# Kernel tuning notes

Measured on AMD Instinct MI355X. Metric: run time of the kernel, lower is better.

## Reference

```python
import jax, jax.numpy as jnp
import numpy as np

C = 256          # embed_dim
NH = 8           # n_heads
NL = 4           # n_levels
NP = 4           # n_points
HD = C // NH     # head dim = 32
SS = np.array([[128, 128], [64, 64], [32, 32], [16, 16]], dtype=np.int64)  # (H_l, W_l)
LSI = np.concatenate([[0], np.cumsum(SS[:, 0] * SS[:, 1])[:-1]]).astype(np.int64)
LIN = int((SS[:, 0] * SS[:, 1]).sum())  # 21760
B = 2
LQ = LIN


def setup_inputs() -> dict:
    key = jax.random.key(0)
    ks = jax.random.split(key, 8)
    s = 0.02
    return {
        "query": jax.random.normal(ks[0], (B, LQ, C), jnp.float32),
        "reference_points": jax.random.uniform(ks[1], (B, LQ, NL, 2), dtype=jnp.float32),
        "input_flatten": jax.random.normal(ks[2], (B, LIN, C), jnp.float32),
        "W_value": jax.random.normal(ks[3], (C, C), jnp.float32) * s,
        "b_value": jnp.zeros((C,), jnp.float32),
        "W_off": jax.random.normal(ks[4], (C, NH * NL * NP * 2), jnp.float32) * s,
        "b_off": jnp.zeros((NH * NL * NP * 2,), jnp.float32),
        "W_attn": jax.random.normal(ks[5], (C, NH * NL * NP), jnp.float32) * s,
        "b_attn": jnp.zeros((NH * NL * NP,), jnp.float32),
        "W_out": jax.random.normal(ks[6], (C, C), jnp.float32) * s,
        "b_out": jnp.zeros((C,), jnp.float32),
        "input_spatial_shapes": jnp.asarray(SS),
        "input_level_start_index": jnp.asarray(LSI),
    }


def _msda(query, reference_points, input_flatten,
          W_value, b_value, W_off, b_off, W_attn, b_attn, W_out, b_out):
    N, Lq, _ = query.shape
    Lin = input_flatten.shape[1]
    # projections
    value = (input_flatten @ W_value + b_value).reshape(N, Lin, NH, HD)
    off = (query @ W_off + b_off).reshape(N, Lq, NH, NL, NP, 2)
    aw = jax.nn.softmax((query @ W_attn + b_attn).reshape(N, Lq, NH, NL * NP), axis=-1)
    aw = aw.reshape(N, Lq, NH, NL, NP)
    # normalizer is (W_l, H_l) per level
    norm = jnp.asarray(SS[:, ::-1].copy(), jnp.float32)  # (NL, 2)
    loc = reference_points[:, :, None, :, None, :] + off / norm[None, None, None, :, None, :]
    out = jnp.zeros((N, Lq, NH, HD), query.dtype)
    for l in range(NL):
        Hl, Wl = int(SS[l, 0]), int(SS[l, 1])
        st = int(LSI[l])
        v = value[:, st:st + Hl * Wl].transpose(0, 2, 1, 3)  # (N, NH, HW, HD)
        # grid_sample align_corners=False semantics: pixel = loc*size - 0.5
        x = loc[:, :, :, l, :, 0] * Wl - 0.5  # (N, Lq, NH, NP)
        y = loc[:, :, :, l, :, 1] * Hl - 0.5
        x0 = jnp.floor(x)
        y0 = jnp.floor(y)
        lw = x - x0
        lh = y - y0
        x0i = x0.astype(jnp.int32)
        y0i = y0.astype(jnp.int32)

        def corner(ix, iy, w):
            valid = (ix >= 0) & (ix < Wl) & (iy >= 0) & (iy < Hl)
            idx = jnp.clip(iy * Wl + ix, 0, Hl * Wl - 1)
            idx_t = idx.transpose(0, 2, 1, 3).reshape(N, NH, Lq * NP)
            g = jnp.take_along_axis(v, idx_t[:, :, :, None], axis=2)
            g = g.reshape(N, NH, Lq, NP, HD)
            wt = (w * valid).transpose(0, 2, 1, 3)  # (N, NH, Lq, NP)
            return g * wt[..., None]

        samp = (corner(x0i, y0i, (1 - lw) * (1 - lh))
                + corner(x0i + 1, y0i, lw * (1 - lh))
                + corner(x0i, y0i + 1, (1 - lw) * lh)
                + corner(x0i + 1, y0i + 1, lw * lh))
        out = out + jnp.einsum('nhqpd,nqhp->nqhd', samp, aw[:, :, :, l])
    return out.reshape(N, Lq, C) @ W_out + b_out


def reference(query, reference_points, input_flatten,
              W_value, b_value, W_off, b_off, W_attn, b_attn, W_out, b_out,
              input_spatial_shapes, input_level_start_index):
    return _msda(query, reference_points, input_flatten,
                 W_value, b_value, W_off, b_off, W_attn, b_attn, W_out, b_out)
```

## Files before the change

### kernel.cpp

```cpp
#include <hip/hip_runtime.h>

typedef unsigned short u16;
typedef unsigned int u32;
typedef short bf16x8 __attribute__((ext_vector_type(8)));
typedef float f32x4 __attribute__((ext_vector_type(4)));

#define LQ_ 21760
#define LIN_ 21760
#define CDIM 256
#define MROWS (2 * LQ_)

__device__ __forceinline__ u16 f2bf(float f) {
  u32 u;
  __builtin_memcpy(&u, &f, 4);
  u32 r = (u + 0x7fffu + ((u >> 16) & 1u)) >> 16;
  return (u16)r;
}
__device__ __forceinline__ u32 pack_bf16_rne(float a, float b) {
  return (u32)f2bf(a) | ((u32)f2bf(b) << 16);
}
__device__ __forceinline__ float bflo(u32 u) {
  u32 v = u << 16;
  float f;
  __builtin_memcpy(&f, &v, 4);
  return f;
}
__device__ __forceinline__ float bfhi(u32 u) {
  u32 v = u & 0xffff0000u;
  float f;
  __builtin_memcpy(&f, &v, 4);
  return f;
}

__device__ __forceinline__ void conv_one(const float* W0, const float* W1, u16* Wf,
                                         int N, int split, int blk, int t) {
  const int tid = blk * 256 + t;
  if (tid >= N * 32) return;
  const int n = tid >> 5, kcg = tid & 31;
  float w[8];
#pragma unroll
  for (int j = 0; j < 8; ++j) {
    const int k = kcg * 8 + j;
    w[j] = (n < split) ? W0[(size_t)k * split + n]
                       : W1[(size_t)k * (N - split) + (n - split)];
  }
  uint4 pk;
  pk.x = pack_bf16_rne(w[0], w[1]);
  pk.y = pack_bf16_rne(w[2], w[3]);
  pk.z = pack_bf16_rne(w[4], w[5]);
  pk.w = pack_bf16_rne(w[6], w[7]);
  const int ks = kcg >> 2, kcr = kcg & 3, c = n >> 4;
  const int chunk = ks * (N / 4) + c * 4 + kcr;
  *(uint4*)(Wf + (size_t)chunk * 128 + (n & 15) * 8) = pk;
}

__global__ __launch_bounds__(256) void conv_fused(
    const float* __restrict__ Wv, const float* __restrict__ Wof,
    const float* __restrict__ Wa, const float* __restrict__ Wo,
    const float* __restrict__ bof, const float* __restrict__ ba,
    u16* __restrict__ WfV, u16* __restrict__ WfC, u16* __restrict__ WfO,
    float* __restrict__ bcat, const float* __restrict__ Aq,
    const float* __restrict__ Ai, u16* __restrict__ Qf, u16* __restrict__ If) {
  const int b = blockIdx.x, t = threadIdx.x;
  if (b < 32) {
    conv_one(Wv, Wv, WfV, 256, 256, b, t);
    return;
  }
  if (b < 80) {
    conv_one(Wof, Wa, WfC, 384, 256, b - 32, t);
    return;
  }
  if (b < 112) {
    conv_one(Wo, Wo, WfO, 256, 256, b - 80, t);
    return;
  }
  if (b < 114) {
    const int i = (b - 112) * 256 + t;
    if (i < 384) bcat[i] = (i < 256) ? bof[i] : ba[i - 256];
    return;
  }
  const int i = (b - 114) * 256 + t;
  const int n4 = MROWS * 32;
  const float* src;
  u16* dst;
  int j;
  if (i < n4) {
    src = Aq;
    dst = Qf;
    j = i;
  } else {
    src = Ai;
    dst = If;
    j = i - n4;
  }
  const int tile = j >> 9;
  const int c2 = (j >> 4) & 31;
  const int sr = j & 15;
  const int row = (tile >> 3) * 128 + (c2 >> 2) * 16 + sr;
  const int kc = (tile & 7) * 32 + (c2 & 3) * 8;
  const float4 f0 = *(const float4*)(src + (size_t)row * 256 + kc);
  const float4 f1 = *(const float4*)(src + (size_t)row * 256 + kc + 4);
  uint4 pk;
  pk.x = pack_bf16_rne(f0.x, f0.y);
  pk.y = pack_bf16_rne(f0.z, f0.w);
  pk.z = pack_bf16_rne(f1.x, f1.y);
  pk.w = pack_bf16_rne(f1.z, f1.w);
  *(uint4*)(dst + (size_t)j * 8) = pk;
}

__global__ __launch_bounds__(256) void gemm_vq(
    const u16* __restrict__ If, const u16* __restrict__ WfV,
    const float* __restrict__ bv, u16* __restrict__ outV,
    const u16* __restrict__ Qf, const u16* __restrict__ WfC,
    const float* __restrict__ bcat, float* __restrict__ outO,
    float* __restrict__ outA) {
  const int t = threadIdx.x, l = t & 63, wv = t >> 6;
  const int wr = wv >> 1, wc = wv & 1;
  const int fq = l >> 4, fr = l & 15;
  bf16x8 af[8][4];

  if (blockIdx.x < 340) {
    const int rb = blockIdx.x;
    const u16* ab = If + (size_t)rb * 32768 + (wr * 16 + fq) * 128 + fr * 8;
#pragma unroll
    for (int ks = 0; ks < 8; ++ks)
#pragma unroll
      for (int r = 0; r < 4; ++r)
        af[ks][r] = *(const bf16x8*)(ab + ks * 4096 + r * 512);
#pragma unroll
    for (int cb = 0; cb < 2; ++cb) {
      f32x4 acc[4][4];
#pragma unroll
      for (int r = 0; r < 4; ++r)
#pragma unroll
        for (int c = 0; c < 4; ++c) acc[r][c] = f32x4{0.f, 0.f, 0.f, 0.f};
      const u16* bb = WfV + ((size_t)(cb * 8 + wc * 4) * 4 + fq) * 128 + fr * 8;
#pragma unroll
      for (int ks = 0; ks < 8; ++ks) {
        bf16x8 bf[4];
#pragma unroll
        for (int c = 0; c < 4; ++c) bf[c] = *(const bf16x8*)(bb + ks * 8192 + c * 512);
#pragma unroll
        for (int c = 0; c < 4; ++c)
#pragma unroll
          for (int r = 0; r < 4; ++r)
            acc[r][c] = __builtin_amdgcn_mfma_f32_16x16x32_bf16(af[ks][r], bf[c],
                                                                acc[r][c], 0, 0, 0);
      }
      const int rq = fq * 4;
#pragma unroll
      for (int c = 0; c < 4; ++c) {
        const int col = cb * 128 + wc * 64 + c * 16 + fr;
        const float bz = bv[col];
#pragma unroll
        for (int r = 0; r < 4; ++r) {
          const int row0 = rb * 128 + wr * 64 + r * 16 + rq;
#pragma unroll
          for (int g = 0; g < 4; ++g)
            outV[(size_t)(row0 + g) * 256 + col] = f2bf(acc[r][c][g] + bz);
        }
      }
    }
  } else {
    const int rb = blockIdx.x - 340;
    const u16* ab = Qf + (size_t)rb * 32768 + (wr * 16 + fq) * 128 + fr * 8;
#pragma unroll
    for (int ks = 0; ks < 8; ++ks)
#pragma unroll
      for (int r = 0; r < 4; ++r)
        af[ks][r] = *(const bf16x8*)(ab + ks * 4096 + r * 512);
#pragma unroll
    for (int cb = 0; cb < 3; ++cb) {
      f32x4 acc[4][4];
#pragma unroll
      for (int r = 0; r < 4; ++r)
#pragma unroll
        for (int c = 0; c < 4; ++c) acc[r][c] = f32x4{0.f, 0.f, 0.f, 0.f};
      const u16* bb = WfC + ((size_t)(cb * 8 + wc * 4) * 4 + fq) * 128 + fr * 8;
#pragma unroll
      for (int ks = 0; ks < 8; ++ks) {
        bf16x8 bf[4];
#pragma unroll
        for (int c = 0; c < 4; ++c) bf[c] = *(const bf16x8*)(bb + ks * 12288 + c * 512);
#pragma unroll
        for (int c = 0; c < 4; ++c)
#pragma unroll
          for (int r = 0; r < 4; ++r)
            acc[r][c] = __builtin_amdgcn_mfma_f32_16x16x32_bf16(af[ks][r], bf[c],
                                                                acc[r][c], 0, 0, 0);
      }
      const int rq = fq * 4;
#pragma unroll
      for (int c = 0; c < 4; ++c) {
        const int col = cb * 128 + wc * 64 + c * 16 + fr;
        const float bz = bcat[col];
#pragma unroll
        for (int r = 0; r < 4; ++r) {
          const int row0 = rb * 128 + wr * 64 + r * 16 + rq;
#pragma unroll
          for (int g = 0; g < 4; ++g) {
            const float v = acc[r][c][g] + bz;
            if (col < 256)
              outO[(size_t)(row0 + g) * 256 + col] = v;
            else
              outA[(size_t)(row0 + g) * 128 + (col - 256)] = v;
          }
        }
      }
    }
  }
}

__global__ __launch_bounds__(256) void gemm_out(
    const u16* __restrict__ A, const u16* __restrict__ Wf,
    const float* __restrict__ bias, float* __restrict__ out) {
  const int rb = blockIdx.x;
  const int t = threadIdx.x, l = t & 63, wv = t >> 6;
  const int wr = wv >> 1, wc = wv & 1;
  const int fq = l >> 4, fr = l & 15;
  bf16x8 af[8][4];
  const u16* ab = A + ((size_t)rb * 128 + wr * 64 + fr) * 256 + fq * 8;
#pragma unroll
  for (int ks = 0; ks < 8; ++ks)
#pragma unroll
    for (int r = 0; r < 4; ++r)
      af[ks][r] = *(const bf16x8*)(ab + (size_t)r * 4096 + ks * 32);
#pragma unroll
  for (int cb = 0; cb < 2; ++cb) {
    f32x4 acc[4][4];
#pragma unroll
    for (int r = 0; r < 4; ++r)
#pragma unroll
      for (int c = 0; c < 4; ++c) acc[r][c] = f32x4{0.f, 0.f, 0.f, 0.f};
    const u16* bb = Wf + ((size_t)(cb * 8 + wc * 4) * 4 + fq) * 128 + fr * 8;
#pragma unroll
    for (int ks = 0; ks < 8; ++ks) {
      bf16x8 bf[4];
#pragma unroll
      for (int c = 0; c < 4; ++c) bf[c] = *(const bf16x8*)(bb + ks * 8192 + c * 512);
#pragma unroll
      for (int c = 0; c < 4; ++c)
#pragma unroll
        for (int r = 0; r < 4; ++r)
          acc[r][c] = __builtin_amdgcn_mfma_f32_16x16x32_bf16(af[ks][r], bf[c],
                                                              acc[r][c], 0, 0, 0);
    }
    const int rq = fq * 4;
#pragma unroll
    for (int c = 0; c < 4; ++c) {
      const int col = cb * 128 + wc * 64 + c * 16 + fr;
      const float bz = bias[col];
#pragma unroll
      for (int r = 0; r < 4; ++r) {
        const int row0 = rb * 128 + wr * 64 + r * 16 + rq;
#pragma unroll
        for (int g = 0; g < 4; ++g)
          out[(size_t)(row0 + g) * 256 + col] = acc[r][c][g] + bz;
      }
    }
  }
}

__global__ __launch_bounds__(256) void msda_sample3(
    const u16* __restrict__ value, const float* __restrict__ off,
    const float* __restrict__ attnl, const float* __restrict__ refp,
    u16* __restrict__ out) {
  __shared__ float s_aw[64 * 17];
  __shared__ uint4 s_idx[16 * 64];
  __shared__ float4 s_w[16 * 64];
  const int t = threadIdx.x;
  const int bq0 = blockIdx.x * 8;

  if (t < 64) {
    const float* lg = attnl + (size_t)(bq0 + (t >> 3)) * 128 + (t & 7) * 16;
    float e[16];
    float m = -1e30f;
#pragma unroll
    for (int i = 0; i < 16; ++i) {
      e[i] = lg[i];
      m = fmaxf(m, e[i]);
    }
    float s = 0.f;
#pragma unroll
    for (int i = 0; i < 16; ++i) {
      e[i] = __expf(e[i] - m);
      s += e[i];
    }
    const float inv = 1.f / s;
#pragma unroll
    for (int i = 0; i < 16; ++i) s_aw[t * 17 + i] = e[i] * inv;
  }
  __syncthreads();

#pragma unroll
  for (int rr = 0; rr < 4; ++rr) {
    const int id = t + rr * 256;
    const int qh = id & 63, lp = id >> 6;
    const int q = qh >> 3, h = qh & 7, lv = lp >> 2, p = lp & 3;
    const int bq = bq0 + q;
    const int Wl = 128 >> lv;
    const int st = (lv == 0) ? 0 : (lv == 1) ? 16384 : (lv == 2) ? 20480 : 21504;
    const float ox = off[(size_t)bq * 256 + ((h * 4 + lv) * 4 + p) * 2];
    const float oy = off[(size_t)bq * 256 + ((h * 4 + lv) * 4 + p) * 2 + 1];
    const float rx = refp[(size_t)bq * 8 + lv * 2];
    const float ry = refp[(size_t)bq * 8 + lv * 2 + 1];
    const float aw = s_aw[qh * 17 + lp];
    const float x = rx * (float)Wl + ox - 0.5f;
    const float y = ry * (float)Wl + oy - 0.5f;
    const float xf = floorf(x), yf = floorf(y);
    const int x0 = (int)xf, y0 = (int)yf;
    const float lw = x - xf, lh = y - yf;
    const float hw = 1.f - lw, hh = 1.f - lh;
    const int ixs[4] = {x0, x0 + 1, x0, x0 + 1};
    const int iys[4] = {y0, y0, y0 + 1, y0 + 1};
    const float wts[4] = {hw * hh, lw * hh, hw * lh, lw * lh};
    u32 rows[4];
    float ws4[4];
#pragma unroll
    for (int c = 0; c < 4; ++c) {
      const int ix = ixs[c], iy = iys[c];
      const bool valid = (ix >= 0) & (ix < Wl) & (iy >= 0) & (iy < Wl);
      int idx = iy * Wl + ix;
      idx = max(0, min(idx, Wl * Wl - 1));
      rows[c] = (u32)(st + idx);
      ws4[c] = valid ? (wts[c] * aw) : 0.f;
    }
    uint4 iv;
    iv.x = rows[0];
    iv.y = rows[1];
    iv.z = rows[2];
    iv.w = rows[3];
    s_idx[lp * 64 + qh] = iv;
    s_w[lp * 64 + qh] = make_float4(ws4[0], ws4[1], ws4[2], ws4[3]);
  }
  __syncthreads();

  const int q = t >> 5, h = (t >> 2) & 7, dg = t & 3;
  const int qh = q * 8 + h;
  const int bq = bq0 + q;
  const u16* vp = value + (size_t)((bq >= LQ_) ? LIN_ : 0) * CDIM + h * 32 + dg * 8;
  float a0 = 0.f, a1 = 0.f, a2 = 0.f, a3 = 0.f;
  float a4 = 0.f, a5 = 0.f, a6 = 0.f, a7 = 0.f;
#pragma unroll 4
  for (int lp = 0; lp < 16; ++lp) {
    const uint4 iv = s_idx[lp * 64 + qh];
    const float4 wv = s_w[lp * 64 + qh];
    const u32 rows[4] = {iv.x, iv.y, iv.z, iv.w};
    const float ww[4] = {wv.x, wv.y, wv.z, wv.w};
#pragma unroll
    for (int c = 0; c < 4; ++c) {
      const uint4 d = *(const uint4*)(vp + (size_t)rows[c] * CDIM);
      const float w = ww[c];
      a0 += w * bflo(d.x);
      a1 += w * bfhi(d.x);
      a2 += w * bflo(d.y);
      a3 += w * bfhi(d.y);
      a4 += w * bflo(d.z);
      a5 += w * bfhi(d.z);
      a6 += w * bflo(d.w);
      a7 += w * bfhi(d.w);
    }
  }
  uint4 o;
  o.x = pack_bf16_rne(a0, a1);
  o.y = pack_bf16_rne(a2, a3);
  o.z = pack_bf16_rne(a4, a5);
  o.w = pack_bf16_rne(a6, a7);
  *(uint4*)(out + (size_t)bq * CDIM + h * 32 + dg * 8) = o;
}

extern "C" void kernel_launch(void* const* d_in, const int* in_sizes, int n_in,
                              void* d_out, int out_size, void* d_ws, size_t ws_size,
                              hipStream_t stream) {
  const float* query = (const float*)d_in[0];
  const float* refp = (const float*)d_in[1];
  const float* inflat = (const float*)d_in[2];
  const float* Wv = (const float*)d_in[3];
  const float* bv = (const float*)d_in[4];
  const float* Wof = (const float*)d_in[5];
  const float* bof = (const float*)d_in[6];
  const float* Wa = (const float*)d_in[7];
  const float* ba = (const float*)d_in[8];
  const float* Wo = (const float*)d_in[9];
  const float* bo = (const float*)d_in[10];
  float* out = (float*)d_out;

  const size_t M = MROWS;

  u16* If = (u16*)d_ws;
  u16* Qf = If + M * 256;
  u16* ws_value = Qf + M * 256;
  float* ws_off = (float*)(ws_value + M * 256);
  float* ws_attn = ws_off + M * 256;
  u16* WfV = (u16*)(ws_attn + M * 128);
  u16* WfC = WfV + 256 * 256;
  u16* WfO = WfC + 384 * 256;
  float* bcat = (float*)(WfO + 256 * 256);
  u16* ws_samp = If;

  conv_fused<<<dim3(10994), dim3(256), 0, stream>>>(Wv, Wof, Wa, Wo, bof, ba, WfV, WfC,
                                                    WfO, bcat, query, inflat, Qf, If);
  gemm_vq<<<dim3(680), dim3(256), 0, stream>>>(If, WfV, bv, ws_value, Qf, WfC, bcat,
                                               ws_off, ws_attn);
  msda_sample3<<<dim3(5440), dim3(256), 0, stream>>>(ws_value, ws_off, ws_attn, refp,
                                                     ws_samp);
  gemm_out<<<dim3(340), dim3(256), 0, stream>>>(ws_samp, WfO, bo, out);
}
```

Before: 285.3 us.

## Fuse fp32-to-bf16 activation conversion into projection GEMM loads; pack sampler indices and math

Removes the separate pass that converted query and input_flatten from fp32 to a pre-tiled bf16 layout. The projection GEMM now reads fp32 rows directly and packs them to bf16 in registers, which drops a full write and re-read of both activation tensors. The sampler also stores its corner indices as 16-bit values in shared memory and accumulates in float2 vectors, which may map to packed FMA instructions. The GEMM's A-operand loads are now strided fp32 reads rather than contiguous pre-swizzled bf16 chunks, so they may coalesce less well.

```diff
diff --git a/kernel.cpp b/kernel.cpp
--- a/kernel.cpp
+++ b/kernel.cpp
@@ -4,6 +4,7 @@
 typedef unsigned int u32;
 typedef short bf16x8 __attribute__((ext_vector_type(8)));
 typedef float f32x4 __attribute__((ext_vector_type(4)));
+typedef float f32x2 __attribute__((ext_vector_type(2)));
 
 #define LQ_ 21760
 #define LIN_ 21760
@@ -19,17 +20,24 @@
 __device__ __forceinline__ u32 pack_bf16_rne(float a, float b) {
   return (u32)f2bf(a) | ((u32)f2bf(b) << 16);
 }
-__device__ __forceinline__ float bflo(u32 u) {
-  u32 v = u << 16;
-  float f;
-  __builtin_memcpy(&f, &v, 4);
-  return f;
-}
-__device__ __forceinline__ float bfhi(u32 u) {
-  u32 v = u & 0xffff0000u;
-  float f;
-  __builtin_memcpy(&f, &v, 4);
-  return f;
+__device__ __forceinline__ f32x2 b2f2(u32 u) {
+  u32 lo = u << 16;
+  u32 hi = u & 0xffff0000u;
+  float fl, fh;
+  __builtin_memcpy(&fl, &lo, 4);
+  __builtin_memcpy(&fh, &hi, 4);
+  return f32x2{fl, fh};
+}
+__device__ __forceinline__ bf16x8 pack8(const float4 a, const float4 b) {
+  union {
+    uint4 u;
+    bf16x8 v;
+  } r;
+  r.u.x = pack_bf16_rne(a.x, a.y);
+  r.u.y = pack_bf16_rne(a.z, a.w);
+  r.u.z = pack_bf16_rne(b.x, b.y);
+  r.u.w = pack_bf16_rne(b.z, b.w);
+  return r.v;
 }
 
 __device__ __forceinline__ void conv_one(const float* W0, const float* W1, u16* Wf,
@@ -54,13 +62,12 @@
   *(uint4*)(Wf + (size_t)chunk * 128 + (n & 15) * 8) = pk;
 }
 
-__global__ __launch_bounds__(256) void conv_fused(
+__global__ __launch_bounds__(256) void conv_w(
     const float* __restrict__ Wv, const float* __restrict__ Wof,
     const float* __restrict__ Wa, const float* __restrict__ Wo,
     const float* __restrict__ bof, const float* __restrict__ ba,
     u16* __restrict__ WfV, u16* __restrict__ WfC, u16* __restrict__ WfO,
-    float* __restrict__ bcat, const float* __restrict__ Aq,
-    const float* __restrict__ Ai, u16* __restrict__ Qf, u16* __restrict__ If) {
+    float* __restrict__ bcat) {
   const int b = blockIdx.x, t = threadIdx.x;
   if (b < 32) {
     conv_one(Wv, Wv, WfV, 256, 256, b, t);
@@ -74,44 +81,14 @@
     conv_one(Wo, Wo, WfO, 256, 256, b - 80, t);
     return;
   }
-  if (b < 114) {
-    const int i = (b - 112) * 256 + t;
-    if (i < 384) bcat[i] = (i < 256) ? bof[i] : ba[i - 256];
-    return;
-  }
-  const int i = (b - 114) * 256 + t;
-  const int n4 = MROWS * 32;
-  const float* src;
-  u16* dst;
-  int j;
-  if (i < n4) {
-    src = Aq;
-    dst = Qf;
-    j = i;
-  } else {
-    src = Ai;
-    dst = If;
-    j = i - n4;
-  }
-  const int tile = j >> 9;
-  const int c2 = (j >> 4) & 31;
-  const int sr = j & 15;
-  const int row = (tile >> 3) * 128 + (c2 >> 2) * 16 + sr;
-  const int kc = (tile & 7) * 32 + (c2 & 3) * 8;
-  const float4 f0 = *(const float4*)(src + (size_t)row * 256 + kc);
-  const float4 f1 = *(const float4*)(src + (size_t)row * 256 + kc + 4);
-  uint4 pk;
-  pk.x = pack_bf16_rne(f0.x, f0.y);
-  pk.y = pack_bf16_rne(f0.z, f0.w);
-  pk.z = pack_bf16_rne(f1.x, f1.y);
-  pk.w = pack_bf16_rne(f1.z, f1.w);
-  *(uint4*)(dst + (size_t)j * 8) = pk;
+  const int i = (b - 112) * 256 + t;
+  if (i < 384) bcat[i] = (i < 256) ? bof[i] : ba[i - 256];
 }
 
 __global__ __launch_bounds__(256) void gemm_vq(
-    const u16* __restrict__ If, const u16* __restrict__ WfV,
+    const float* __restrict__ Ai, const u16* __restrict__ WfV,
     const float* __restrict__ bv, u16* __restrict__ outV,
-    const u16* __restrict__ Qf, const u16* __restrict__ WfC,
+    const float* __restrict__ Aq, const u16* __restrict__ WfC,
     const float* __restrict__ bcat, float* __restrict__ outO,
     float* __restrict__ outA) {
   const int t = threadIdx.x, l = t & 63, wv = t >> 6;
@@ -121,12 +98,15 @@
 
   if (blockIdx.x < 340) {
     const int rb = blockIdx.x;
-    const u16* ab = If + (size_t)rb * 32768 + (wr * 16 + fq) * 128 + fr * 8;
+    const float* ab = Ai + (size_t)(rb * 128 + wr * 64 + fr) * 256 + fq * 8;
 #pragma unroll
     for (int ks = 0; ks < 8; ++ks)
 #pragma unroll
-      for (int r = 0; r < 4; ++r)
-        af[ks][r] = *(const bf16x8*)(ab + ks * 4096 + r * 512);
+      for (int r = 0; r < 4; ++r) {
+        const float4 f0 = *(const float4*)(ab + (size_t)r * 4096 + ks * 32);
+        const float4 f1 = *(const float4*)(ab + (size_t)r * 4096 + ks * 32 + 4);
+        af[ks][r] = pack8(f0, f1);
+      }
 #pragma unroll
     for (int cb = 0; cb < 2; ++cb) {
       f32x4 acc[4][4];
@@ -163,12 +143,15 @@
     }
   } else {
     const int rb = blockIdx.x - 340;
-    const u16* ab = Qf + (size_t)rb * 32768 + (wr * 16 + fq) * 128 + fr * 8;
+    const float* ab = Aq + (size_t)(rb * 128 + wr * 64 + fr) * 256 + fq * 8;
 #pragma unroll
     for (int ks = 0; ks < 8; ++ks)
 #pragma unroll
-      for (int r = 0; r < 4; ++r)
-        af[ks][r] = *(const bf16x8*)(ab + ks * 4096 + r * 512);
+      for (int r = 0; r < 4; ++r) {
+        const float4 f0 = *(const float4*)(ab + (size_t)r * 4096 + ks * 32);
+        const float4 f1 = *(const float4*)(ab + (size_t)r * 4096 + ks * 32 + 4);
+        af[ks][r] = pack8(f0, f1);
+      }
 #pragma unroll
     for (int cb = 0; cb < 3; ++cb) {
       f32x4 acc[4][4];
@@ -261,12 +244,12 @@
   }
 }
 
-__global__ __launch_bounds__(256) void msda_sample3(
+__global__ __launch_bounds__(256) void msda_sample4(
     const u16* __restrict__ value, const float* __restrict__ off,
     const float* __restrict__ attnl, const float* __restrict__ refp,
     u16* __restrict__ out) {
   __shared__ float s_aw[64 * 17];
-  __shared__ uint4 s_idx[16 * 64];
+  __shared__ ushort4 s_idx[16 * 64];
   __shared__ float4 s_w[16 * 64];
   const int t = threadIdx.x;
   const int bq0 = blockIdx.x * 8;
@@ -325,11 +308,11 @@
       rows[c] = (u32)(st + idx);
       ws4[c] = valid ? (wts[c] * aw) : 0.f;
     }
-    uint4 iv;
-    iv.x = rows[0];
-    iv.y = rows[1];
-    iv.z = rows[2];
-    iv.w = rows[3];
+    ushort4 iv;
+    iv.x = (u16)rows[0];
+    iv.y = (u16)rows[1];
+    iv.z = (u16)rows[2];
+    iv.w = (u16)rows[3];
     s_idx[lp * 64 + qh] = iv;
     s_w[lp * 64 + qh] = make_float4(ws4[0], ws4[1], ws4[2], ws4[3]);
   }
@@ -339,11 +322,10 @@
   const int qh = q * 8 + h;
   const int bq = bq0 + q;
   const u16* vp = value + (size_t)((bq >= LQ_) ? LIN_ : 0) * CDIM + h * 32 + dg * 8;
-  float a0 = 0.f, a1 = 0.f, a2 = 0.f, a3 = 0.f;
-  float a4 = 0.f, a5 = 0.f, a6 = 0.f, a7 = 0.f;
+  f32x2 a0 = {0.f, 0.f}, a1 = {0.f, 0.f}, a2 = {0.f, 0.f}, a3 = {0.f, 0.f};
 #pragma unroll 4
   for (int lp = 0; lp < 16; ++lp) {
-    const uint4 iv = s_idx[lp * 64 + qh];
+    const ushort4 iv = s_idx[lp * 64 + qh];
     const float4 wv = s_w[lp * 64 + qh];
     const u32 rows[4] = {iv.x, iv.y, iv.z, iv.w};
     const float ww[4] = {wv.x, wv.y, wv.z, wv.w};
@@ -351,21 +333,18 @@
     for (int c = 0; c < 4; ++c) {
       const uint4 d = *(const uint4*)(vp + (size_t)rows[c] * CDIM);
       const float w = ww[c];
-      a0 += w * bflo(d.x);
-      a1 += w * bfhi(d.x);
-      a2 += w * bflo(d.y);
-      a3 += w * bfhi(d.y);
-      a4 += w * bflo(d.z);
-      a5 += w * bfhi(d.z);
-      a6 += w * bflo(d.w);
-      a7 += w * bfhi(d.w);
+      const f32x2 w2 = {w, w};
+      a0 += w2 * b2f2(d.x);
+      a1 += w2 * b2f2(d.y);
+      a2 += w2 * b2f2(d.z);
+      a3 += w2 * b2f2(d.w);
     }
   }
   uint4 o;
-  o.x = pack_bf16_rne(a0, a1);
-  o.y = pack_bf16_rne(a2, a3);
-  o.z = pack_bf16_rne(a4, a5);
-  o.w = pack_bf16_rne(a6, a7);
+  o.x = pack_bf16_rne(a0[0], a0[1]);
+  o.y = pack_bf16_rne(a1[0], a1[1]);
+  o.z = pack_bf16_rne(a2[0], a2[1]);
+  o.w = pack_bf16_rne(a3[0], a3[1]);
   *(uint4*)(out + (size_t)bq * CDIM + h * 32 + dg * 8) = o;
 }
 
@@ -387,22 +366,20 @@
 
   const size_t M = MROWS;
 
-  u16* If = (u16*)d_ws;
-  u16* Qf = If + M * 256;
-  u16* ws_value = Qf + M * 256;
+  u16* ws_value = (u16*)d_ws;
   float* ws_off = (float*)(ws_value + M * 256);
   float* ws_attn = ws_off + M * 256;
   u16* WfV = (u16*)(ws_attn + M * 128);
   u16* WfC = WfV + 256 * 256;
   u16* WfO = WfC + 384 * 256;
   float* bcat = (float*)(WfO + 256 * 256);
-  u16* ws_samp = If;
-
-  conv_fused<<<dim3(10994), dim3(256), 0, stream>>>(Wv, Wof, Wa, Wo, bof, ba, WfV, WfC,
-                                                    WfO, bcat, query, inflat, Qf, If);
-  gemm_vq<<<dim3(680), dim3(256), 0, stream>>>(If, WfV, bv, ws_value, Qf, WfC, bcat,
-                                               ws_off, ws_attn);
-  msda_sample3<<<dim3(5440), dim3(256), 0, stream>>>(ws_value, ws_off, ws_attn, refp,
+  u16* ws_samp = (u16*)(bcat + 384);
+
+  conv_w<<<dim3(114), dim3(256), 0, stream>>>(Wv, Wof, Wa, Wo, bof, ba, WfV, WfC, WfO,
+                                              bcat);
+  gemm_vq<<<dim3(680), dim3(256), 0, stream>>>(inflat, WfV, bv, ws_value, query, WfC,
+                                               bcat, ws_off, ws_attn);
+  msda_sample4<<<dim3(5440), dim3(256), 0, stream>>>(ws_value, ws_off, ws_attn, refp,
                                                      ws_samp);
   gemm_out<<<dim3(340), dim3(256), 0, stream>>>(ws_samp, WfO, bo, out);
 }
```

After: 310.5 us. 8.8% more time.

## Fuse fp32-to-bf16 activation conversion into GEMM via swizzled LDS staging

Applied to the files above, without the earlier changes.

Removes the separate pass that converted query and input_flatten to a pre-tiled bf16 layout. The GEMMs now load fp32 rows directly, convert them, and stage them in a 64KB XOR-swizzled shared-memory tile. A-fragments are read from LDS per k-step instead of being held in registers. This cuts one full read-and-write pass over both activations and lowers register pressure, but raises LDS use to 64KB per block, which may limit occupancy. gemm_out also moves to LDS staging, and ws_samp now gets its own buffer.

```diff
diff --git a/kernel.cpp b/kernel.cpp
--- a/kernel.cpp
+++ b/kernel.cpp
@@ -54,13 +54,12 @@
   *(uint4*)(Wf + (size_t)chunk * 128 + (n & 15) * 8) = pk;
 }
 
-__global__ __launch_bounds__(256) void conv_fused(
+__global__ __launch_bounds__(256) void conv_w(
     const float* __restrict__ Wv, const float* __restrict__ Wof,
     const float* __restrict__ Wa, const float* __restrict__ Wo,
     const float* __restrict__ bof, const float* __restrict__ ba,
     u16* __restrict__ WfV, u16* __restrict__ WfC, u16* __restrict__ WfO,
-    float* __restrict__ bcat, const float* __restrict__ Aq,
-    const float* __restrict__ Ai, u16* __restrict__ Qf, u16* __restrict__ If) {
+    float* __restrict__ bcat) {
   const int b = blockIdx.x, t = threadIdx.x;
   if (b < 32) {
     conv_one(Wv, Wv, WfV, 256, 256, b, t);
@@ -74,59 +73,53 @@
     conv_one(Wo, Wo, WfO, 256, 256, b - 80, t);
     return;
   }
-  if (b < 114) {
-    const int i = (b - 112) * 256 + t;
-    if (i < 384) bcat[i] = (i < 256) ? bof[i] : ba[i - 256];
-    return;
-  }
-  const int i = (b - 114) * 256 + t;
-  const int n4 = MROWS * 32;
-  const float* src;
-  u16* dst;
-  int j;
-  if (i < n4) {
-    src = Aq;
-    dst = Qf;
-    j = i;
-  } else {
-    src = Ai;
-    dst = If;
-    j = i - n4;
-  }
-  const int tile = j >> 9;
-  const int c2 = (j >> 4) & 31;
-  const int sr = j & 15;
-  const int row = (tile >> 3) * 128 + (c2 >> 2) * 16 + sr;
-  const int kc = (tile & 7) * 32 + (c2 & 3) * 8;
-  const float4 f0 = *(const float4*)(src + (size_t)row * 256 + kc);
-  const float4 f1 = *(const float4*)(src + (size_t)row * 256 + kc + 4);
-  uint4 pk;
-  pk.x = pack_bf16_rne(f0.x, f0.y);
-  pk.y = pack_bf16_rne(f0.z, f0.w);
-  pk.z = pack_bf16_rne(f1.x, f1.y);
-  pk.w = pack_bf16_rne(f1.z, f1.w);
-  *(uint4*)(dst + (size_t)j * 8) = pk;
+  const int i = (b - 112) * 256 + t;
+  if (i < 384) bcat[i] = (i < 256) ? bof[i] : ba[i - 256];
+}
+
+__device__ __forceinline__ void stage_a_f32(u16* s_a, const float* __restrict__ ga,
+                                            int t) {
+#pragma unroll
+  for (int it = 0; it < 16; ++it) {
+    const int idx = it * 256 + t;
+    const int row = idx >> 5, cc = idx & 31;
+    const float4 f0 = *(const float4*)(ga + (size_t)row * 256 + cc * 8);
+    const float4 f1 = *(const float4*)(ga + (size_t)row * 256 + cc * 8 + 4);
+    uint4 pk;
+    pk.x = pack_bf16_rne(f0.x, f0.y);
+    pk.y = pack_bf16_rne(f0.z, f0.w);
+    pk.z = pack_bf16_rne(f1.x, f1.y);
+    pk.w = pack_bf16_rne(f1.z, f1.w);
+    *(uint4*)(s_a + row * 256 + ((cc * 8) ^ ((row & 7) << 3))) = pk;
+  }
+}
+__device__ __forceinline__ void stage_a_bf16(u16* s_a, const u16* __restrict__ ga,
+                                             int t) {
+#pragma unroll
+  for (int it = 0; it < 16; ++it) {
+    const int idx = it * 256 + t;
+    const int row = idx >> 5, cc = idx & 31;
+    const uint4 pk = *(const uint4*)(ga + (size_t)row * 256 + cc * 8);
+    *(uint4*)(s_a + row * 256 + ((cc * 8) ^ ((row & 7) << 3))) = pk;
+  }
 }
 
 __global__ __launch_bounds__(256) void gemm_vq(
-    const u16* __restrict__ If, const u16* __restrict__ WfV,
+    const float* __restrict__ Ai, const u16* __restrict__ WfV,
     const float* __restrict__ bv, u16* __restrict__ outV,
-    const u16* __restrict__ Qf, const u16* __restrict__ WfC,
+    const float* __restrict__ Aq, const u16* __restrict__ WfC,
     const float* __restrict__ bcat, float* __restrict__ outO,
     float* __restrict__ outA) {
+  __shared__ u16 s_a[128 * 256];
   const int t = threadIdx.x, l = t & 63, wv = t >> 6;
   const int wr = wv >> 1, wc = wv & 1;
   const int fq = l >> 4, fr = l & 15;
-  bf16x8 af[8][4];
+  const int swz = (fr & 7) << 3;
 
   if (blockIdx.x < 340) {
     const int rb = blockIdx.x;
-    const u16* ab = If + (size_t)rb * 32768 + (wr * 16 + fq) * 128 + fr * 8;
-#pragma unroll
-    for (int ks = 0; ks < 8; ++ks)
-#pragma unroll
-      for (int r = 0; r < 4; ++r)
-        af[ks][r] = *(const bf16x8*)(ab + ks * 4096 + r * 512);
+    stage_a_f32(s_a, Ai + (size_t)rb * 128 * 256, t);
+    __syncthreads();
 #pragma unroll
     for (int cb = 0; cb < 2; ++cb) {
       f32x4 acc[4][4];
@@ -137,6 +130,12 @@
       const u16* bb = WfV + ((size_t)(cb * 8 + wc * 4) * 4 + fq) * 128 + fr * 8;
 #pragma unroll
       for (int ks = 0; ks < 8; ++ks) {
+        bf16x8 af[4];
+#pragma unroll
+        for (int r = 0; r < 4; ++r) {
+          const int row = wr * 64 + r * 16 + fr;
+          af[r] = *(const bf16x8*)(s_a + row * 256 + ((ks * 32 + fq * 8) ^ swz));
+        }
         bf16x8 bf[4];
 #pragma unroll
         for (int c = 0; c < 4; ++c) bf[c] = *(const bf16x8*)(bb + ks * 8192 + c * 512);
@@ -144,7 +143,7 @@
         for (int c = 0; c < 4; ++c)
 #pragma unroll
           for (int r = 0; r < 4; ++r)
-            acc[r][c] = __builtin_amdgcn_mfma_f32_16x16x32_bf16(af[ks][r], bf[c],
+            acc[r][c] = __builtin_amdgcn_mfma_f32_16x16x32_bf16(af[r], bf[c],
                                                                 acc[r][c], 0, 0, 0);
       }
       const int rq = fq * 4;
@@ -163,12 +162,8 @@
     }
   } else {
     const int rb = blockIdx.x - 340;
-    const u16* ab = Qf + (size_t)rb * 32768 + (wr * 16 + fq) * 128 + fr * 8;
-#pragma unroll
-    for (int ks = 0; ks < 8; ++ks)
-#pragma unroll
-      for (int r = 0; r < 4; ++r)
-        af[ks][r] = *(const bf16x8*)(ab + ks * 4096 + r * 512);
+    stage_a_f32(s_a, Aq + (size_t)rb * 128 * 256, t);
+    __syncthreads();
 #pragma unroll
     for (int cb = 0; cb < 3; ++cb) {
       f32x4 acc[4][4];
@@ -179,6 +174,12 @@
       const u16* bb = WfC + ((size_t)(cb * 8 + wc * 4) * 4 + fq) * 128 + fr * 8;
 #pragma unroll
       for (int ks = 0; ks < 8; ++ks) {
+        bf16x8 af[4];
+#pragma unroll
+        for (int r = 0; r < 4; ++r) {
+          const int row = wr * 64 + r * 16 + fr;
+          af[r] = *(const bf16x8*)(s_a + row * 256 + ((ks * 32 + fq * 8) ^ swz));
+        }
         bf16x8 bf[4];
 #pragma unroll
         for (int c = 0; c < 4; ++c) bf[c] = *(const bf16x8*)(bb + ks * 12288 + c * 512);
@@ -186,7 +187,7 @@
         for (int c = 0; c < 4; ++c)
 #pragma unroll
           for (int r = 0; r < 4; ++r)
-            acc[r][c] = __builtin_amdgcn_mfma_f32_16x16x32_bf16(af[ks][r], bf[c],
+            acc[r][c] = __builtin_amdgcn_mfma_f32_16x16x32_bf16(af[r], bf[c],
                                                                 acc[r][c], 0, 0, 0);
       }
       const int rq = fq * 4;
@@ -214,17 +215,14 @@
 __global__ __launch_bounds__(256) void gemm_out(
     const u16* __restrict__ A, const u16* __restrict__ Wf,
     const float* __restrict__ bias, float* __restrict__ out) {
+  __shared__ u16 s_a[128 * 256];
   const int rb = blockIdx.x;
   const int t = threadIdx.x, l = t & 63, wv = t >> 6;
   const int wr = wv >> 1, wc = wv & 1;
   const int fq = l >> 4, fr = l & 15;
-  bf16x8 af[8][4];
-  const u16* ab = A + ((size_t)rb * 128 + wr * 64 + fr) * 256 + fq * 8;
-#pragma unroll
-  for (int ks = 0; ks < 8; ++ks)
-#pragma unroll
-    for (int r = 0; r < 4; ++r)
-      af[ks][r] = *(const bf16x8*)(ab + (size_t)r * 4096 + ks * 32);
+  const int swz = (fr & 7) << 3;
+  stage_a_bf16(s_a, A + (size_t)rb * 128 * 256, t);
+  __syncthreads();
 #pragma unroll
   for (int cb = 0; cb < 2; ++cb) {
     f32x4 acc[4][4];
@@ -235,6 +233,12 @@
     const u16* bb = Wf + ((size_t)(cb * 8 + wc * 4) * 4 + fq) * 128 + fr * 8;
 #pragma unroll
     for (int ks = 0; ks < 8; ++ks) {
+      bf16x8 af[4];
+#pragma unroll
+      for (int r = 0; r < 4; ++r) {
+        const int row = wr * 64 + r * 16 + fr;
+        af[r] = *(const bf16x8*)(s_a + row * 256 + ((ks * 32 + fq * 8) ^ swz));
+      }
       bf16x8 bf[4];
 #pragma unroll
       for (int c = 0; c < 4; ++c) bf[c] = *(const bf16x8*)(bb + ks * 8192 + c * 512);
@@ -242,7 +246,7 @@
       for (int c = 0; c < 4; ++c)
 #pragma unroll
         for (int r = 0; r < 4; ++r)
-          acc[r][c] = __builtin_amdgcn_mfma_f32_16x16x32_bf16(af[ks][r], bf[c],
+          acc[r][c] = __builtin_amdgcn_mfma_f32_16x16x32_bf16(af[r], bf[c],
                                                               acc[r][c], 0, 0, 0);
     }
     const int rq = fq * 4;
@@ -387,21 +391,19 @@
 
   const size_t M = MROWS;
 
-  u16* If = (u16*)d_ws;
-  u16* Qf = If + M * 256;
-  u16* ws_value = Qf + M * 256;
+  u16* ws_value = (u16*)d_ws;
   float* ws_off = (float*)(ws_value + M * 256);
   float* ws_attn = ws_off + M * 256;
-  u16* WfV = (u16*)(ws_attn + M * 128);
+  u16* ws_samp = (u16*)(ws_attn + M * 128);
+  u16* WfV = ws_samp + M * 256;
   u16* WfC = WfV + 256 * 256;
   u16* WfO = WfC + 384 * 256;
   float* bcat = (float*)(WfO + 256 * 256);
-  u16* ws_samp = If;
-
-  conv_fused<<<dim3(10994), dim3(256), 0, stream>>>(Wv, Wof, Wa, Wo, bof, ba, WfV, WfC,
-                                                    WfO, bcat, query, inflat, Qf, If);
-  gemm_vq<<<dim3(680), dim3(256), 0, stream>>>(If, WfV, bv, ws_value, Qf, WfC, bcat,
-                                               ws_off, ws_attn);
+
+  conv_w<<<dim3(114), dim3(256), 0, stream>>>(Wv, Wof, Wa, Wo, bof, ba, WfV, WfC, WfO,
+                                              bcat);
+  gemm_vq<<<dim3(680), dim3(256), 0, stream>>>(inflat, WfV, bv, ws_value, query, WfC,
+                                               bcat, ws_off, ws_attn);
   msda_sample3<<<dim3(5440), dim3(256), 0, stream>>>(ws_value, ws_off, ws_attn, refp,
                                                      ws_samp);
   gemm_out<<<dim3(340), dim3(256), 0, stream>>>(ws_samp, WfO, bo, out);
```

New measurement: 286.9 us. No clear change (+0.5%).
